# Optimization experiments

Hardware: AMD Instinct MI355X
Metric: run time of the kernel (lower is better)

## Reference

```python
import jax, jax.numpy as jnp
import numpy as np

N = 50000
E = 800000
IN_DIM = 128
HIDDEN = 128
OUT_DIM = 64
NUM_GRAPHS = 64


def setup_inputs() -> dict:
    key = jax.random.key(0)
    ks = jax.random.split(key, 16)
    x = jax.random.normal(ks[0], (N, IN_DIM), dtype=jnp.float32)
    edge_index = jax.random.randint(ks[1], (2, E), 0, N, dtype=jnp.int32)
    batch = jnp.sort(jax.random.randint(ks[2], (N,), 0, NUM_GRAPHS, dtype=jnp.int32))

    def glorot(k, shape):
        fan_in = shape[1]
        return jax.random.normal(k, shape, dtype=jnp.float32) / jnp.sqrt(jnp.float32(fan_in))

    # SAGEConv params: lin_l (on aggregated neighbors, with bias), lin_r (on self, no bias)
    return {
        "x": x,
        "edge_index": edge_index,
        "batch": batch,
        "W1l": glorot(ks[3], (HIDDEN, IN_DIM)), "b1l": jnp.zeros((HIDDEN,), jnp.float32),
        "W1r": glorot(ks[4], (HIDDEN, IN_DIM)),
        "W2l": glorot(ks[5], (HIDDEN, HIDDEN)), "b2l": jnp.zeros((HIDDEN,), jnp.float32),
        "W2r": glorot(ks[6], (HIDDEN, HIDDEN)),
        "W3l": glorot(ks[7], (HIDDEN, HIDDEN)), "b3l": jnp.zeros((HIDDEN,), jnp.float32),
        "W3r": glorot(ks[8], (HIDDEN, HIDDEN)),
        "Wlin": glorot(ks[9], (OUT_DIM, HIDDEN)), "blin": jnp.zeros((OUT_DIM,), jnp.float32),
    }


def sage_conv(x, src, dst, Wl, bl, Wr):
    # aggr='add': scatter-add source features onto target nodes, then two linears.
    agg = jax.ops.segment_sum(x[src], dst, num_segments=N)  # [N, d_in]
    return agg @ Wl.T + bl + x @ Wr.T


def reference(x, edge_index, batch, W1l, b1l, W1r, W2l, b2l, W2r, W3l, b3l, W3r, Wlin, blin):
    src, dst = edge_index[0], edge_index[1]
    h = jax.nn.relu(sage_conv(x, src, dst, W1l, b1l, W1r))
    # dropout p=0.3 is identity at inference
    h = jax.nn.relu(sage_conv(h, src, dst, W2l, b2l, W2r))
    h = sage_conv(h, src, dst, W3l, b3l, W3r)
    # global mean pool over graphs
    sums = jax.ops.segment_sum(h, batch, num_segments=NUM_GRAPHS)  # [G, hidden]
    counts = jax.ops.segment_sum(jnp.ones((N,), h.dtype), batch, num_segments=NUM_GRAPHS)
    pooled = sums / jnp.maximum(counts, 1.0)[:, None]
    return pooled @ Wlin.T + blin  # [G, out_dim]
```

## Files before the change

### kernel.cpp

```cpp
#include <hip/hip_runtime.h>


typedef __bf16 bf16x8 __attribute__((ext_vector_type(8)));
typedef float f32x4 __attribute__((ext_vector_type(4)));
typedef float f32x2 __attribute__((ext_vector_type(2)));

#define BINB 160
#define NBMAX 512

static __device__ __forceinline__ unsigned short f2bf(float f) {
    unsigned u = __builtin_bit_cast(unsigned, f);
    return (unsigned short)((u + 0x7fffu + ((u >> 16) & 1u)) >> 16);
}
static __device__ __forceinline__ uint2 pk8_fp8(const float* f) {
    int lo = 0, hi = 0;
    lo = __builtin_amdgcn_cvt_pk_fp8_f32(f[0], f[1], lo, false);
    lo = __builtin_amdgcn_cvt_pk_fp8_f32(f[2], f[3], lo, true);
    hi = __builtin_amdgcn_cvt_pk_fp8_f32(f[4], f[5], hi, false);
    hi = __builtin_amdgcn_cvt_pk_fp8_f32(f[6], f[7], hi, true);
    return make_uint2((unsigned)lo, (unsigned)hi);
}
static __device__ __forceinline__ unsigned char f2fp8(float v) {
    return (unsigned char)(__builtin_amdgcn_cvt_pk_fp8_f32(v, v, 0, false) & 0xff);
}

__global__ __launch_bounds__(256) void k_bincast(
    const int* __restrict__ ei, int* __restrict__ cnt_mat, int E, int nb, int epb,
    const float* __restrict__ x, unsigned short* __restrict__ xb,
    unsigned char* __restrict__ x8, int n8, int nxblk,
    const float* __restrict__ W1l, const float* __restrict__ W1r,
    const float* __restrict__ W2l, const float* __restrict__ W2r,
    unsigned short* __restrict__ Whi,
    const int* __restrict__ batch, unsigned* __restrict__ cnt, int nsp, int hepb)
{
    __shared__ int lc[NBMAX];
    int bid = blockIdx.x;
    if (bid < BINB) {
        for (int i = threadIdx.x; i < nb; i += 256) lc[i] = 0;
        __syncthreads();
        int b0 = bid * epb;
        int b1 = min(b0 + epb, E);
        for (int i = b0 + threadIdx.x; i < b1; i += 256)
            atomicAdd(&lc[ei[E + i] >> 7], 1);
        __syncthreads();
        for (int i = threadIdx.x; i < nb; i += 256)
            cnt_mat[i * BINB + bid] = lc[i];
    } else if (bid < BINB + nxblk) {
        int i = (bid - BINB) * 256 + threadIdx.x;
        if (i >= n8) return;
        float f[8];
        *(float4*)(f + 0) = *(const float4*)(x + (size_t)i * 8);
        *(float4*)(f + 4) = *(const float4*)(x + (size_t)i * 8 + 4);
        ushort4 oa, ob;
        oa.x = f2bf(f[0]); oa.y = f2bf(f[1]); oa.z = f2bf(f[2]); oa.w = f2bf(f[3]);
        ob.x = f2bf(f[4]); ob.y = f2bf(f[5]); ob.z = f2bf(f[6]); ob.w = f2bf(f[7]);
        int node = i >> 4, c = i & 15;
        size_t dstb = (size_t)(node >> 4) * 2048 + (size_t)(c >> 2) * 512
                    + (size_t)((c & 3) * 16 + (node & 15)) * 8;
        *(ushort4*)(xb + dstb) = oa;
        *(ushort4*)(xb + dstb + 4) = ob;
        *(uint2*)(x8 + (size_t)i * 8) = pk8_fp8(f);
    } else if (bid < BINB + nxblk + 256) {
        int wb = bid - BINB - nxblk;
        int layer = wb >> 7;
        int j = wb & 127;
        int k = threadIdx.x;
        const float* Wl = (layer == 0) ? W1l : W2l;
        const float* Wr = (layer == 0) ? W1r : W2r;
        float w = (k < 128) ? Wl[j * 128 + k] : Wr[j * 128 + k - 128];
        int js = j >> 4, mr = j & 15;
        int s = k >> 5, quad = (k >> 3) & 3, e = k & 7;
        size_t o = (size_t)layer * 32768
                 + ((size_t)(js * 8 + s) * 64 + quad * 16 + mr) * 8 + e;
        Whi[o] = f2bf(w);
    } else {
        int hb = bid - BINB - nxblk - 256;
        int b0 = hb * hepb;
        int b1 = min(b0 + hepb, E);
        for (int i = b0 + threadIdx.x; i < b1; i += 256) {
            int s = ei[i];
            int d = ei[E + i];
            int g = batch[d];
            atomicAdd(&cnt[(size_t)g * nsp + s], 1u);
        }
    }
}

__global__ __launch_bounds__(256) void k_mrowscan(
    const int* __restrict__ cnt_mat, int* __restrict__ rowloc, int* __restrict__ btot)
{
    __shared__ int s[256];
    int b = blockIdx.x;
    int t = threadIdx.x;
    int v = (t < BINB) ? cnt_mat[b * BINB + t] : 0;
    s[t] = v;
    __syncthreads();
#pragma unroll
    for (int off = 1; off < 256; off <<= 1) {
        int u = (t >= off) ? s[t - off] : 0;
        __syncthreads();
        s[t] += u;
        __syncthreads();
    }
    if (t < BINB) rowloc[b * BINB + t] = s[t] - v;
    if (t == 255) btot[b] = s[255];
}

__global__ __launch_bounds__(256) void k_scan2b(
    const int* __restrict__ btot, int* __restrict__ bbase, int nb, int* __restrict__ total_out)
{
    __shared__ int s[256];
    int t = threadIdx.x;
    int per = (nb + 255) / 256;
    int s0 = t * per, e0 = min(s0 + per, nb);
    int sum = 0;
    for (int i = s0; i < e0; ++i) sum += btot[i];
    s[t] = sum;
    __syncthreads();
#pragma unroll
    for (int off = 1; off < 256; off <<= 1) {
        int u = (t >= off) ? s[t - off] : 0;
        __syncthreads();
        s[t] += u;
        __syncthreads();
    }
    int run = s[t] - sum;
    for (int i = s0; i < e0; ++i) { bbase[i] = run; run += btot[i]; }
    if (t == 255) *total_out = s[255];
}

__global__ __launch_bounds__(256) void k_binscatter(
    const int* __restrict__ ei, const int* __restrict__ rowloc, const int* __restrict__ bbase,
    unsigned* __restrict__ binned, int E, int nb, int epb)
{
    __shared__ int lofs[NBMAX];
    __shared__ int lcnt[NBMAX];
    for (int i = threadIdx.x; i < nb; i += 256) {
        lofs[i] = rowloc[i * BINB + blockIdx.x] + bbase[i];
        lcnt[i] = 0;
    }
    __syncthreads();
    int b0 = blockIdx.x * epb;
    int b1 = min(b0 + epb, E);
    for (int i = b0 + threadIdx.x; i < b1; i += 256) {
        int s = ei[i];
        int d = ei[E + i];
        int b = d >> 7;
        int r = atomicAdd(&lcnt[b], 1);
        binned[lofs[b] + r] = (unsigned)s | ((unsigned)(d & 127) << 16);
    }
}

__global__ __launch_bounds__(256) void k_fillfine2(
    const unsigned* __restrict__ binned, const int* __restrict__ bbase,
    const int* __restrict__ batch, int* __restrict__ starts,
    unsigned short* __restrict__ csr_src, int* __restrict__ gestart,
    int E, int nb, int n)
{
    __shared__ int lc[128];
    __shared__ int lpos[128];
    int b = blockIdx.x;
    int t = threadIdx.x;
    int node0 = b << 7;
    int bs = bbase[b];
    int be = (b == nb - 1) ? E : bbase[b + 1];
    if (t < 128) lc[t] = 0;
    __syncthreads();
    for (int i = bs + t; i < be; i += 256)
        atomicAdd(&lc[(binned[i] >> 16) & 127], 1);
    __syncthreads();
    int v = (t < 128) ? lc[t] : 0;
    if (t < 128) lpos[t] = v;
    __syncthreads();
#pragma unroll
    for (int off = 1; off < 128; off <<= 1) {
        int u = (t >= off && t < 128) ? lpos[t - off] : 0;
        __syncthreads();
        if (t < 128) lpos[t] += u;
        __syncthreads();
    }
    int excl = (t < 128) ? (lpos[t] - v) : 0;
    __syncthreads();
    if (t < 128) {
        int node = node0 + t;
        if (node < n) {
            int st = bs + excl;
            starts[node] = st;
            int bc = batch[node];
            int bp = (node == 0) ? -1 : batch[node - 1];
            for (int g = bp + 1; g <= bc; ++g) gestart[g] = st;
            if (node == n - 1)
                for (int g = bc + 1; g <= 64; ++g) gestart[g] = E;
        }
        lpos[t] = bs + excl;
    }
    if (b == nb - 1 && t == 0) starts[n] = E;
    __syncthreads();
    for (int i = bs + t; i < be; i += 256) {
        unsigned e = binned[i];
        int slot = atomicAdd(&lpos[(e >> 16) & 127], 1);
        csr_src[slot] = (unsigned short)(e & 0xffffu);
    }
}

#define ACC8P(v)                                                        \
    do {                                                                \
        f32x2 p0 = __builtin_amdgcn_cvt_pk_f32_fp8((v).x, false);       \
        f32x2 p1 = __builtin_amdgcn_cvt_pk_f32_fp8((v).x, true);        \
        f32x2 p2 = __builtin_amdgcn_cvt_pk_f32_fp8((v).y, false);       \
        f32x2 p3 = __builtin_amdgcn_cvt_pk_f32_fp8((v).y, true);        \
        A01 += p0; A23 += p1; A45 += p2; A67 += p3;                     \
    } while (0)

#define PROC_CHUNK(idxv, cntv)                                          \
    {                                                                   \
        int j = 0;                                                      \
        for (; j + 16 <= (cntv); j += 16) {                             \
            int s0 = __shfl((int)(idxv), j + eg);                       \
            int s1 = __shfl((int)(idxv), j + 4 + eg);                   \
            int s2 = __shfl((int)(idxv), j + 8 + eg);                   \
            int s3 = __shfl((int)(idxv), j + 12 + eg);                  \
            uint2 v0 = *(const uint2*)(hrow + (size_t)s0 * 128);        \
            uint2 v1 = *(const uint2*)(hrow + (size_t)s1 * 128);        \
            uint2 v2 = *(const uint2*)(hrow + (size_t)s2 * 128);        \
            uint2 v3 = *(const uint2*)(hrow + (size_t)s3 * 128);        \
            ACC8P(v0);                                                  \
            ACC8P(v1);                                                  \
            ACC8P(v2);                                                  \
            ACC8P(v3);                                                  \
        }                                                               \
        for (; j + 4 <= (cntv); j += 4) {                               \
            int s0 = __shfl((int)(idxv), j + eg);                       \
            uint2 v0 = *(const uint2*)(hrow + (size_t)s0 * 128);        \
            ACC8P(v0);                                                  \
        }                                                               \
        if (j < (cntv)) {                                               \
            int k = j + eg;                                             \
            int sm = __shfl((int)(idxv), (k < (cntv)) ? k : ((cntv) - 1)); \
            uint2 v = *(const uint2*)(hrow + (size_t)sm * 128);         \
            if (k >= (cntv)) v = make_uint2(0u, 0u);                    \
            ACC8P(v);                                                   \
        }                                                               \
    }

#define REDUCE8()                                                       \
    a0 += __shfl_xor(a0, 16); a0 += __shfl_xor(a0, 32);                 \
    a1 += __shfl_xor(a1, 16); a1 += __shfl_xor(a1, 32);                 \
    a2 += __shfl_xor(a2, 16); a2 += __shfl_xor(a2, 32);                 \
    a3 += __shfl_xor(a3, 16); a3 += __shfl_xor(a3, 32);                 \
    a4 += __shfl_xor(a4, 16); a4 += __shfl_xor(a4, 32);                 \
    a5 += __shfl_xor(a5, 16); a5 += __shfl_xor(a5, 32);                 \
    a6 += __shfl_xor(a6, 16); a6 += __shfl_xor(a6, 32);                 \
    a7 += __shfl_xor(a7, 16); a7 += __shfl_xor(a7, 32);

__global__ __launch_bounds__(256) void k_layer(
    const unsigned char* __restrict__ h8_in, const int* __restrict__ starts,
    const unsigned short* __restrict__ csr, const unsigned short* __restrict__ hf,
    const unsigned short* __restrict__ Whi, const float* __restrict__ bl,
    unsigned short* __restrict__ outf, unsigned char* __restrict__ out8,
    unsigned char* __restrict__ h2t,
    int n, int nsp, int do_outf, int do_h2t)
{
    __shared__ unsigned short sagg[2048];
    int t = threadIdx.x;
    int wv = t >> 6;
    int lane = t & 63;
    int node0 = blockIdx.x * 16;

    {
        int eg = lane >> 4;
        int fb = lane & 15;
        const unsigned char* hrow = h8_in + fb * 8;
        int nodeA = node0 + wv * 4;
        int st[5];
#pragma unroll
        for (int r = 0; r < 5; ++r) {
            int nn = nodeA + r;
            st[r] = starts[nn > n ? n : nn];
        }
        unsigned idx4[4];
#pragma unroll
        for (int r = 0; r < 4; ++r)
            idx4[r] = (st[r] + lane < st[r + 1]) ? (unsigned)csr[st[r] + lane] : 0u;

#pragma unroll
        for (int r = 0; r < 4; ++r) {
            int node = nodeA + r;
            if (node >= n) break;
            f32x2 A01 = (f32x2){0.f, 0.f}, A23 = (f32x2){0.f, 0.f},
                  A45 = (f32x2){0.f, 0.f}, A67 = (f32x2){0.f, 0.f};
            int deg = st[r + 1] - st[r];
            int c0 = min(64, deg);
            PROC_CHUNK(idx4[r], c0)
            for (int base = st[r] + 64; base < st[r + 1]; base += 64) {
                int cnt2 = min(64, st[r + 1] - base);
                unsigned idx = (base + lane < st[r + 1]) ? (unsigned)csr[base + lane] : 0u;
                PROC_CHUNK(idx, cnt2)
            }
            float a0 = A01.x, a1 = A01.y, a2 = A23.x, a3 = A23.y,
                  a4 = A45.x, a5 = A45.y, a6 = A67.x, a7 = A67.y;
            REDUCE8()
            if (eg == 0) {
                int ln = node - node0;
                unsigned u0 = (unsigned)f2bf(a0) | ((unsigned)f2bf(a1) << 16);
                unsigned u1 = (unsigned)f2bf(a2) | ((unsigned)f2bf(a3) << 16);
                unsigned u2 = (unsigned)f2bf(a4) | ((unsigned)f2bf(a5) << 16);
                unsigned u3 = (unsigned)f2bf(a6) | ((unsigned)f2bf(a7) << 16);
                size_t dst = (size_t)(fb >> 2) * 512 + (size_t)((fb & 3) * 16 + ln) * 8;
                *(uint4*)(sagg + dst) = make_uint4(u0, u1, u2, u3);
            }
        }
    }
    __syncthreads();

    int quad = lane >> 4;
    int mr = lane & 15;
    int js0 = wv * 2;

    f32x4 acc0 = (f32x4){0.f, 0.f, 0.f, 0.f};
    f32x4 acc1 = (f32x4){0.f, 0.f, 0.f, 0.f};

    const unsigned short* wp = Whi + (size_t)js0 * 4096 + (size_t)lane * 8;
    const unsigned short* sa = sagg + (size_t)lane * 8;
    const unsigned short* ha = hf + (size_t)blockIdx.x * 2048 + (size_t)lane * 8;

    uint4 pb[2][3];
#define LAYER_LOAD(s, b)                                                  \
    do {                                                                  \
        pb[b][0] = *(const uint4*)(wp + (size_t)(s) * 512);               \
        pb[b][1] = *(const uint4*)(wp + 4096 + (size_t)(s) * 512);        \
        pb[b][2] = ((s) < 4)                                              \
            ? *(const uint4*)(sa + (size_t)(s) * 512)                     \
            : *(const uint4*)(ha + (size_t)((s) - 4) * 512);              \
    } while (0)

    LAYER_LOAD(0, 0);
    LAYER_LOAD(1, 1);
#pragma unroll
    for (int s = 0; s < 8; ++s) {
        int b = s & 1;
        bf16x8 bh0 = __builtin_bit_cast(bf16x8, pb[b][0]);
        bf16x8 bh1 = __builtin_bit_cast(bf16x8, pb[b][1]);
        bf16x8 A0 = __builtin_bit_cast(bf16x8, pb[b][2]);
        acc0 = __builtin_amdgcn_mfma_f32_16x16x32_bf16(A0, bh0, acc0, 0, 0, 0);
        acc1 = __builtin_amdgcn_mfma_f32_16x16x32_bf16(A0, bh1, acc1, 0, 0, 0);
        if (s + 2 < 8) LAYER_LOAD(s + 2, b);
    }
#undef LAYER_LOAD

#pragma unroll
    for (int mi = 0; mi < 2; ++mi) {
        f32x4 a = mi ? acc1 : acc0;
        int col = (js0 + mi) * 16 + mr;
        float bias = bl[col];
        int q2 = (col >> 3) & 3;
        int e2 = col & 7;
        int so = col >> 5;
        float vr[4];
#pragma unroll
        for (int r = 0; r < 4; ++r) {
            int node = node0 + quad * 4 + r;
            float v = a[r] + bias;
            v = fmaxf(v, 0.f);
            vr[r] = (node < n) ? v : 0.f;
            if (node < n) {
                if (do_outf)
                    outf[(size_t)(node >> 4) * 2048 + (size_t)so * 512
                         + (size_t)(q2 * 16 + (node & 15)) * 8 + e2] = f2bf(v);
                out8[(size_t)node * 128 + col] = f2fp8(v);
            }
        }
        if (do_h2t) {
            int pk = __builtin_amdgcn_cvt_pk_fp8_f32(vr[0], vr[1], 0, false);
            pk = __builtin_amdgcn_cvt_pk_fp8_f32(vr[2], vr[3], pk, true);
            *(unsigned*)(h2t + (size_t)col * nsp + node0 + quad * 4) = (unsigned)pk;
        }
    }
}

__global__ __launch_bounds__(256) void k_gsum(
    const unsigned* __restrict__ cnt, const unsigned char* __restrict__ h2t,
    const unsigned char* __restrict__ h8, const int* __restrict__ batch,
    float* __restrict__ gsumE, float* __restrict__ gsumP,
    int n, int nsp, int ksteps, int gb)
{
    int t = threadIdx.x;
    if ((int)blockIdx.x >= gb) {
        int wave = ((blockIdx.x - gb) * 256 + t) >> 6;
        int lane = t & 63;
        int r0 = wave * 16;
        if (r0 >= n) return;
        int r1 = min(r0 + 16, n);
        int cur = batch[r0];
        float ax = 0.f, ay = 0.f;
        for (int i = r0; i < r1; ++i) {
            int g = batch[i];
            uchar2 v = *(const uchar2*)(h8 + (size_t)i * 128 + lane * 2);
            if (g != cur) {
                atomicAdd(&gsumP[cur * 128 + lane * 2], ax);
                atomicAdd(&gsumP[cur * 128 + lane * 2 + 1], ay);
                ax = 0.f; ay = 0.f; cur = g;
            }
            unsigned pk = (unsigned)v.x | ((unsigned)v.y << 8);
            f32x2 p = __builtin_amdgcn_cvt_pk_f32_fp8((int)pk, false);
            ax += p.x;
            ay += p.y;
        }
        atomicAdd(&gsumP[cur * 128 + lane * 2], ax);
        atomicAdd(&gsumP[cur * 128 + lane * 2 + 1], ay);
        return;
    }

    int wv = t >> 6;
    int lane = t & 63;
    int fast = lane & 15;
    int kc = (lane >> 4) * 8;
    int kpb = (ksteps + gb - 1) / gb;
    int k0 = blockIdx.x * kpb, k1 = min(k0 + kpb, ksteps);
    if (k0 >= k1) return;

    f32x4 acc[8];
#pragma unroll
    for (int i = 0; i < 8; ++i) acc[i] = (f32x4){0.f, 0.f, 0.f, 0.f};

    const unsigned* ap = cnt + (size_t)(wv * 16 + fast) * nsp + kc;
    const unsigned char* bp = h2t + (size_t)fast * nsp + kc;

    for (int ks = k0; ks < k1; ++ks) {
        int kb = ks * 32;
        uint4 c0 = *(const uint4*)(ap + kb);
        uint4 c1 = *(const uint4*)(ap + kb + 4);
        unsigned q0 = (unsigned)f2bf((float)c0.x) | ((unsigned)f2bf((float)c0.y) << 16);
        unsigned q1 = (unsigned)f2bf((float)c0.z) | ((unsigned)f2bf((float)c0.w) << 16);
        unsigned q2 = (unsigned)f2bf((float)c1.x) | ((unsigned)f2bf((float)c1.y) << 16);
        unsigned q3 = (unsigned)f2bf((float)c1.z) | ((unsigned)f2bf((float)c1.w) << 16);
        uint4 au = make_uint4(q0, q1, q2, q3);
        bf16x8 af = __builtin_bit_cast(bf16x8, au);
#pragma unroll
        for (int ft = 0; ft < 8; ++ft) {
            uint2 bb = *(const uint2*)(bp + (size_t)ft * 16 * nsp + kb);
            f32x2 p0 = __builtin_amdgcn_cvt_pk_f32_fp8(bb.x, false);
            f32x2 p1 = __builtin_amdgcn_cvt_pk_f32_fp8(bb.x, true);
            f32x2 p2 = __builtin_amdgcn_cvt_pk_f32_fp8(bb.y, false);
            f32x2 p3 = __builtin_amdgcn_cvt_pk_f32_fp8(bb.y, true);
            unsigned b0 = (unsigned)f2bf(p0.x) | ((unsigned)f2bf(p0.y) << 16);
            unsigned b1 = (unsigned)f2bf(p1.x) | ((unsigned)f2bf(p1.y) << 16);
            unsigned b2 = (unsigned)f2bf(p2.x) | ((unsigned)f2bf(p2.y) << 16);
            unsigned b3 = (unsigned)f2bf(p3.x) | ((unsigned)f2bf(p3.y) << 16);
            uint4 bu = make_uint4(b0, b1, b2, b3);
            bf16x8 bf = __builtin_bit_cast(bf16x8, bu);
            acc[ft] = __builtin_amdgcn_mfma_f32_16x16x32_bf16(af, bf, acc[ft], 0, 0, 0);
        }
    }

    int quad = lane >> 4;
    int mr = lane & 15;
    int gg = wv * 16 + quad * 4;
#pragma unroll
    for (int ft = 0; ft < 8; ++ft) {
        int col = ft * 16 + mr;
#pragma unroll
        for (int r = 0; r < 4; ++r)
            atomicAdd(&gsumE[(size_t)(gg + r) * 128 + col], acc[ft][r]);
    }
}

__global__ __launch_bounds__(128) void k_final(
    const float* __restrict__ gsumE, const float* __restrict__ gsumP,
    const int* __restrict__ batch,
    const float* __restrict__ W3l, const float* __restrict__ b3,
    const float* __restrict__ W3r,
    const float* __restrict__ Wlin, const float* __restrict__ blin,
    float* __restrict__ out, int n)
{
    __shared__ float tmp[128];
    int g = blockIdx.x;
    int t = threadIdx.x;
    int lo = 0, hi = n;
    while (lo < hi) { int m = (lo + hi) >> 1; if (batch[m] < g) lo = m + 1; else hi = m; }
    int lb = lo;
    hi = n;
    while (lo < hi) { int m = (lo + hi) >> 1; if (batch[m] < g + 1) lo = m + 1; else hi = m; }
    int cnt = lo - lb;
    float inv = (cnt > 0) ? 1.f / (float)cnt : 0.f;

    float acc = 0.f;
    for (int k = 0; k < 128; ++k)
        acc += gsumE[g * 128 + k] * W3l[t * 128 + k]
             + gsumP[g * 128 + k] * W3r[t * 128 + k];
    tmp[t] = acc * inv + ((cnt > 0) ? b3[t] : 0.f);
    __syncthreads();

    if (t < 64) {
        float o = 0.f;
        for (int k = 0; k < 128; ++k)
            o += tmp[k] * Wlin[t * 128 + k];
        out[g * 64 + t] = o + blin[t];
    }
}

extern "C" void kernel_launch(void* const* d_in, const int* in_sizes, int n_in,
                              void* d_out, int out_size, void* d_ws, size_t ws_size,
                              hipStream_t stream) {
    const float* x     = (const float*)d_in[0];
    const int*   ei    = (const int*)d_in[1];
    const int*   batch = (const int*)d_in[2];
    const float* W1l = (const float*)d_in[3];
    const float* b1l = (const float*)d_in[4];
    const float* W1r = (const float*)d_in[5];
    const float* W2l = (const float*)d_in[6];
    const float* b2l = (const float*)d_in[7];
    const float* W2r = (const float*)d_in[8];
    const float* W3l = (const float*)d_in[9];
    const float* b3l = (const float*)d_in[10];
    const float* W3r = (const float*)d_in[11];
    const float* Wlin = (const float*)d_in[12];
    const float* blin = (const float*)d_in[13];

    const int N = in_sizes[2];
    const int E = in_sizes[1] / 2;
    const int nb = (N + 127) >> 7;
    const int epb = (E + BINB - 1) / BINB;
    const int NSP = ((N + 16 + 31) / 32) * 32;
    const int KSTEPS = NSP / 32;

    size_t off = 0;
    auto alloc = [&](size_t bytes) {
        void* p = (char*)d_ws + off;
        off += (bytes + 255) & ~(size_t)255;
        return p;
    };
    int* csr_start = (int*)alloc((size_t)(N + 1) * 4);
    int* cnt_mat   = (int*)alloc((size_t)nb * BINB * 4);
    int* rowloc    = (int*)alloc((size_t)nb * BINB * 4);
    int* btot      = (int*)alloc((size_t)NBMAX * 4);
    int* bbase     = (int*)alloc((size_t)NBMAX * 4);
    int* gestart   = (int*)alloc(256 + 64);
    unsigned short* csr_src = (unsigned short*)alloc((size_t)E * 2);
    unsigned*       binned  = (unsigned*)alloc((size_t)E * 4);
    unsigned short* x_bf = (unsigned short*)alloc((size_t)N * 128 * 2 + 65536);
    unsigned short* hA   = (unsigned short*)alloc((size_t)N * 128 * 2 + 65536);
    unsigned char*  x8   = (unsigned char*)alloc((size_t)N * 128);
    unsigned char*  h1_8 = (unsigned char*)alloc((size_t)N * 128);
    unsigned char*  h2_8 = (unsigned char*)alloc((size_t)N * 128);
    unsigned char*  h2T  = (unsigned char*)alloc((size_t)128 * NSP);
    unsigned short* Whi = (unsigned short*)alloc(2 * 128 * 256 * 2);
    unsigned* cnt  = (unsigned*)alloc((size_t)64 * NSP * 4);
    float* gsumE = (float*)alloc((size_t)64 * 128 * 4);
    float* gsumP = (float*)alloc((size_t)64 * 128 * 4);
    (void)ws_size;

    hipMemsetAsync(cnt, 0, (size_t)64 * NSP * 4 + (size_t)2 * 64 * 128 * 4, stream);

    int n8 = N * 128 / 8;
    int nxblk = (n8 + 255) / 256;
    const int HISTB = 256;
    int hepb = (E + HISTB - 1) / HISTB;
    k_bincast<<<BINB + nxblk + 256 + HISTB, 256, 0, stream>>>(
        ei, cnt_mat, E, nb, epb,
        x, x_bf, x8, n8, nxblk, W1l, W1r, W2l, W2r, Whi,
        batch, cnt, NSP, hepb);
    k_mrowscan<<<nb, 256, 0, stream>>>(cnt_mat, rowloc, btot);
    k_scan2b<<<1, 256, 0, stream>>>(btot, bbase, nb, csr_start + N);
    k_binscatter<<<BINB, 256, 0, stream>>>(ei, rowloc, bbase, binned, E, nb, epb);
    k_fillfine2<<<nb, 256, 0, stream>>>(binned, bbase, batch, csr_start, csr_src,
                                        gestart, E, nb, N);

    int lay_grid  = (N + 15) / 16;
    int lay2_grid = NSP / 16;
    int pool_grid = (((N + 15) / 16) + 3) / 4;
    const int GB = 256;

    k_layer<<<lay_grid, 256, 0, stream>>>(x8, csr_start, csr_src, x_bf,
                                          Whi, b1l, hA, h1_8, h2T, N, NSP, 1, 0);
    k_layer<<<lay2_grid, 256, 0, stream>>>(h1_8, csr_start, csr_src, hA,
                                           Whi + 32768, b2l, hA, h2_8, h2T, N, NSP, 0, 1);
    k_gsum<<<GB + pool_grid, 256, 0, stream>>>(cnt, h2T, h2_8, batch,
                                               gsumE, gsumP, N, NSP, KSTEPS, GB);

    k_final<<<64, 128, 0, stream>>>(gsumE, gsumP, batch, W3l, b3l, W3r,
                                    Wlin, blin, (float*)d_out, N);
}
```

Baseline: 288.1 us.

## Build graph-pool count matrix in LDS histograms and fold self-pool into bf16 GEMM

Replaces the global-atomic (graph, source) edge histogram with a per-graph, per-chunk LDS histogram kernel that reads the sorted CSR and writes bf16 counts directly. It also adds a one-hot batch matrix, so the self-feature pooling becomes a second MFMA in the same GEMM. Layer outputs are staged through shared memory for coalesced stores, and layer 2 now writes bf16 transposed features. The pooling GEMM prefetches operands and writes per-block partials, which the final kernel reduces instead of using float atomics. This removes the memset and global atomics but adds a 128xNSP bf16 count buffer, a larger partials buffer, and a serial reduction over 128 partials in the final kernel.

```diff
diff --git a/kernel.cpp b/kernel.cpp
--- a/kernel.cpp
+++ b/kernel.cpp
@@ -7,6 +7,7 @@
 
 #define BINB 160
 #define NBMAX 512
+#define CH 8192
 
 static __device__ __forceinline__ unsigned short f2bf(float f) {
     unsigned u = __builtin_bit_cast(unsigned, f);
@@ -30,8 +31,7 @@
     unsigned char* __restrict__ x8, int n8, int nxblk,
     const float* __restrict__ W1l, const float* __restrict__ W1r,
     const float* __restrict__ W2l, const float* __restrict__ W2r,
-    unsigned short* __restrict__ Whi,
-    const int* __restrict__ batch, unsigned* __restrict__ cnt, int nsp, int hepb)
+    unsigned short* __restrict__ Whi)
 {
     __shared__ int lc[NBMAX];
     int bid = blockIdx.x;
@@ -60,7 +60,7 @@
         *(ushort4*)(xb + dstb) = oa;
         *(ushort4*)(xb + dstb + 4) = ob;
         *(uint2*)(x8 + (size_t)i * 8) = pk8_fp8(f);
-    } else if (bid < BINB + nxblk + 256) {
+    } else {
         int wb = bid - BINB - nxblk;
         int layer = wb >> 7;
         int j = wb & 127;
@@ -73,16 +73,6 @@
         size_t o = (size_t)layer * 32768
                  + ((size_t)(js * 8 + s) * 64 + quad * 16 + mr) * 8 + e;
         Whi[o] = f2bf(w);
-    } else {
-        int hb = bid - BINB - nxblk - 256;
-        int b0 = hb * hepb;
-        int b1 = min(b0 + hepb, E);
-        for (int i = b0 + threadIdx.x; i < b1; i += 256) {
-            int s = ei[i];
-            int d = ei[E + i];
-            int g = batch[d];
-            atomicAdd(&cnt[(size_t)g * nsp + s], 1u);
-        }
     }
 }
 
@@ -200,6 +190,42 @@
         unsigned e = binned[i];
         int slot = atomicAdd(&lpos[(e >> 16) & 127], 1);
         csr_src[slot] = (unsigned short)(e & 0xffffu);
+    }
+}
+
+__global__ __launch_bounds__(256) void k_hist(
+    const unsigned short* __restrict__ csr, const int* __restrict__ gestart,
+    const int* __restrict__ batch, unsigned short* __restrict__ cntb,
+    int n, int nsp, int nch)
+{
+    __shared__ unsigned lc[CH];
+    int bid = blockIdx.x;
+    int c = bid % nch;
+    int gr = bid / nch;
+    int s0 = c * CH;
+    int t = threadIdx.x;
+    if (gr < 64) {
+        for (int i = t; i < CH; i += 256) lc[i] = 0;
+        __syncthreads();
+        int e0 = gestart[gr], e1 = gestart[gr + 1];
+        for (int i = e0 + t; i < e1; i += 256) {
+            unsigned d = (unsigned)((int)csr[i] - s0);
+            if (d < (unsigned)CH) atomicAdd(&lc[d], 1u);
+        }
+        __syncthreads();
+        for (int i = t; i < CH; i += 256) {
+            int s = s0 + i;
+            if (s < nsp)
+                cntb[(size_t)gr * nsp + s] = f2bf((float)lc[i]);
+        }
+    } else {
+        int g2 = gr - 64;
+        for (int i = t; i < CH; i += 256) {
+            int s = s0 + i;
+            if (s < nsp)
+                cntb[(size_t)gr * nsp + s] =
+                    (s < n && batch[s] == g2) ? (unsigned short)0x3f80 : (unsigned short)0;
+        }
     }
 }
 
@@ -258,10 +284,11 @@
     const unsigned short* __restrict__ csr, const unsigned short* __restrict__ hf,
     const unsigned short* __restrict__ Whi, const float* __restrict__ bl,
     unsigned short* __restrict__ outf, unsigned char* __restrict__ out8,
-    unsigned char* __restrict__ h2t,
-    int n, int nsp, int do_outf, int do_h2t)
+    unsigned short* __restrict__ h2tb,
+    int n, int nsp, int mode)
 {
     __shared__ unsigned short sagg[2048];
+    __shared__ unsigned char s8[2048];
     int t = threadIdx.x;
     int wv = t >> 6;
     int lane = t & 63;
@@ -348,134 +375,137 @@
     }
 #undef LAYER_LOAD
 
+    float vv[2][4];
 #pragma unroll
     for (int mi = 0; mi < 2; ++mi) {
         f32x4 a = mi ? acc1 : acc0;
         int col = (js0 + mi) * 16 + mr;
         float bias = bl[col];
-        int q2 = (col >> 3) & 3;
-        int e2 = col & 7;
-        int so = col >> 5;
-        float vr[4];
 #pragma unroll
         for (int r = 0; r < 4; ++r) {
             int node = node0 + quad * 4 + r;
-            float v = a[r] + bias;
-            v = fmaxf(v, 0.f);
-            vr[r] = (node < n) ? v : 0.f;
-            if (node < n) {
-                if (do_outf)
-                    outf[(size_t)(node >> 4) * 2048 + (size_t)so * 512
-                         + (size_t)(q2 * 16 + (node & 15)) * 8 + e2] = f2bf(v);
-                out8[(size_t)node * 128 + col] = f2fp8(v);
+            float v = fmaxf(a[r] + bias, 0.f);
+            vv[mi][r] = (node < n) ? v : 0.f;
+        }
+    }
+    __syncthreads();
+    if (mode == 0) {
+#pragma unroll
+        for (int mi = 0; mi < 2; ++mi) {
+            int col = (js0 + mi) * 16 + mr;
+            int so = col >> 5, q2 = (col >> 3) & 3, e2 = col & 7;
+#pragma unroll
+            for (int r = 0; r < 4; ++r) {
+                int nl = quad * 4 + r;
+                sagg[so * 512 + (q2 * 16 + nl) * 8 + e2] = f2bf(vv[mi][r]);
+                s8[nl * 128 + col] = f2fp8(vv[mi][r]);
             }
         }
-        if (do_h2t) {
-            int pk = __builtin_amdgcn_cvt_pk_fp8_f32(vr[0], vr[1], 0, false);
-            pk = __builtin_amdgcn_cvt_pk_fp8_f32(vr[2], vr[3], pk, true);
-            *(unsigned*)(h2t + (size_t)col * nsp + node0 + quad * 4) = (unsigned)pk;
-        }
+        __syncthreads();
+        *(uint4*)(outf + (size_t)blockIdx.x * 2048 + (size_t)t * 8) =
+            *(const uint4*)(sagg + (size_t)t * 8);
+        int nl = t >> 4;
+        if (node0 + nl < n)
+            *(uint2*)(out8 + (size_t)(node0 + nl) * 128 + (t & 15) * 8) =
+                *(const uint2*)(s8 + nl * 128 + (t & 15) * 8);
+    } else {
+#pragma unroll
+        for (int mi = 0; mi < 2; ++mi) {
+            int col = (js0 + mi) * 16 + mr;
+#pragma unroll
+            for (int r = 0; r < 4; ++r)
+                sagg[col * 16 + quad * 4 + r] = f2bf(vv[mi][r]);
+        }
+        __syncthreads();
+        int col = t >> 1;
+        *(uint4*)(h2tb + (size_t)col * nsp + node0 + (t & 1) * 8) =
+            *(const uint4*)(sagg + col * 16 + (t & 1) * 8);
     }
 }
 
 __global__ __launch_bounds__(256) void k_gsum(
-    const unsigned* __restrict__ cnt, const unsigned char* __restrict__ h2t,
-    const unsigned char* __restrict__ h8, const int* __restrict__ batch,
-    float* __restrict__ gsumE, float* __restrict__ gsumP,
-    int n, int nsp, int ksteps, int gb)
+    const unsigned short* __restrict__ cntb, const unsigned short* __restrict__ h2tb,
+    float* __restrict__ part, int nsp, int ksteps, int gb)
 {
     int t = threadIdx.x;
-    if ((int)blockIdx.x >= gb) {
-        int wave = ((blockIdx.x - gb) * 256 + t) >> 6;
-        int lane = t & 63;
-        int r0 = wave * 16;
-        if (r0 >= n) return;
-        int r1 = min(r0 + 16, n);
-        int cur = batch[r0];
-        float ax = 0.f, ay = 0.f;
-        for (int i = r0; i < r1; ++i) {
-            int g = batch[i];
-            uchar2 v = *(const uchar2*)(h8 + (size_t)i * 128 + lane * 2);
-            if (g != cur) {
-                atomicAdd(&gsumP[cur * 128 + lane * 2], ax);
-                atomicAdd(&gsumP[cur * 128 + lane * 2 + 1], ay);
-                ax = 0.f; ay = 0.f; cur = g;
-            }
-            unsigned pk = (unsigned)v.x | ((unsigned)v.y << 8);
-            f32x2 p = __builtin_amdgcn_cvt_pk_f32_fp8((int)pk, false);
-            ax += p.x;
-            ay += p.y;
-        }
-        atomicAdd(&gsumP[cur * 128 + lane * 2], ax);
-        atomicAdd(&gsumP[cur * 128 + lane * 2 + 1], ay);
-        return;
-    }
-
-    int wv = t >> 6;
-    int lane = t & 63;
+    int wv = t >> 6, lane = t & 63;
     int fast = lane & 15;
     int kc = (lane >> 4) * 8;
     int kpb = (ksteps + gb - 1) / gb;
     int k0 = blockIdx.x * kpb, k1 = min(k0 + kpb, ksteps);
-    if (k0 >= k1) return;
-
-    f32x4 acc[8];
-#pragma unroll
-    for (int i = 0; i < 8; ++i) acc[i] = (f32x4){0.f, 0.f, 0.f, 0.f};
-
-    const unsigned* ap = cnt + (size_t)(wv * 16 + fast) * nsp + kc;
-    const unsigned char* bp = h2t + (size_t)fast * nsp + kc;
-
-    for (int ks = k0; ks < k1; ++ks) {
-        int kb = ks * 32;
-        uint4 c0 = *(const uint4*)(ap + kb);
-        uint4 c1 = *(const uint4*)(ap + kb + 4);
-        unsigned q0 = (unsigned)f2bf((float)c0.x) | ((unsigned)f2bf((float)c0.y) << 16);
-        unsigned q1 = (unsigned)f2bf((float)c0.z) | ((unsigned)f2bf((float)c0.w) << 16);
-        unsigned q2 = (unsigned)f2bf((float)c1.x) | ((unsigned)f2bf((float)c1.y) << 16);
-        unsigned q3 = (unsigned)f2bf((float)c1.z) | ((unsigned)f2bf((float)c1.w) << 16);
-        uint4 au = make_uint4(q0, q1, q2, q3);
-        bf16x8 af = __builtin_bit_cast(bf16x8, au);
-#pragma unroll
-        for (int ft = 0; ft < 8; ++ft) {
-            uint2 bb = *(const uint2*)(bp + (size_t)ft * 16 * nsp + kb);
-            f32x2 p0 = __builtin_amdgcn_cvt_pk_f32_fp8(bb.x, false);
-            f32x2 p1 = __builtin_amdgcn_cvt_pk_f32_fp8(bb.x, true);
-            f32x2 p2 = __builtin_amdgcn_cvt_pk_f32_fp8(bb.y, false);
-            f32x2 p3 = __builtin_amdgcn_cvt_pk_f32_fp8(bb.y, true);
-            unsigned b0 = (unsigned)f2bf(p0.x) | ((unsigned)f2bf(p0.y) << 16);
-            unsigned b1 = (unsigned)f2bf(p1.x) | ((unsigned)f2bf(p1.y) << 16);
-            unsigned b2 = (unsigned)f2bf(p2.x) | ((unsigned)f2bf(p2.y) << 16);
-            unsigned b3 = (unsigned)f2bf(p3.x) | ((unsigned)f2bf(p3.y) << 16);
-            uint4 bu = make_uint4(b0, b1, b2, b3);
-            bf16x8 bf = __builtin_bit_cast(bf16x8, bu);
-            acc[ft] = __builtin_amdgcn_mfma_f32_16x16x32_bf16(af, bf, acc[ft], 0, 0, 0);
-        }
-    }
-
-    int quad = lane >> 4;
-    int mr = lane & 15;
-    int gg = wv * 16 + quad * 4;
+
+    f32x4 accE[8], accP[8];
+#pragma unroll
+    for (int i = 0; i < 8; ++i) {
+        accE[i] = (f32x4){0.f, 0.f, 0.f, 0.f};
+        accP[i] = (f32x4){0.f, 0.f, 0.f, 0.f};
+    }
+
+    const unsigned short* apE = cntb + (size_t)(wv * 16 + fast) * nsp + kc;
+    const unsigned short* apP = apE + (size_t)64 * nsp;
+    const unsigned short* bp  = h2tb + (size_t)fast * nsp + kc;
+
+    if (k0 < k1) {
+        int kb = k0 * 32;
+        uint4 ca0 = *(const uint4*)(apE + kb);
+        uint4 ca1 = *(const uint4*)(apP + kb);
+        uint4 cb[8];
+#pragma unroll
+        for (int ft = 0; ft < 8; ++ft)
+            cb[ft] = *(const uint4*)(bp + (size_t)ft * 16 * nsp + kb);
+        for (int ks = k0; ks < k1; ++ks) {
+            int kn = min(ks + 1, k1 - 1) * 32;
+            uint4 na0 = *(const uint4*)(apE + kn);
+            uint4 na1 = *(const uint4*)(apP + kn);
+            uint4 nb[8];
+#pragma unroll
+            for (int ft = 0; ft < 8; ++ft)
+                nb[ft] = *(const uint4*)(bp + (size_t)ft * 16 * nsp + kn);
+            bf16x8 aE = __builtin_bit_cast(bf16x8, ca0);
+            bf16x8 aP = __builtin_bit_cast(bf16x8, ca1);
+#pragma unroll
+            for (int ft = 0; ft < 8; ++ft) {
+                bf16x8 bf = __builtin_bit_cast(bf16x8, cb[ft]);
+                accE[ft] = __builtin_amdgcn_mfma_f32_16x16x32_bf16(aE, bf, accE[ft], 0, 0, 0);
+                accP[ft] = __builtin_amdgcn_mfma_f32_16x16x32_bf16(aP, bf, accP[ft], 0, 0, 0);
+            }
+            ca0 = na0; ca1 = na1;
+#pragma unroll
+            for (int ft = 0; ft < 8; ++ft) cb[ft] = nb[ft];
+        }
+    }
+    float* po = part + (size_t)blockIdx.x * 16384;
+    int quad = lane >> 4, mr = lane & 15;
 #pragma unroll
     for (int ft = 0; ft < 8; ++ft) {
         int col = ft * 16 + mr;
 #pragma unroll
-        for (int r = 0; r < 4; ++r)
-            atomicAdd(&gsumE[(size_t)(gg + r) * 128 + col], acc[ft][r]);
+        for (int r = 0; r < 4; ++r) {
+            po[(size_t)(wv * 16 + quad * 4 + r) * 128 + col] = accE[ft][r];
+            po[(size_t)(64 + wv * 16 + quad * 4 + r) * 128 + col] = accP[ft][r];
+        }
     }
 }
 
 __global__ __launch_bounds__(128) void k_final(
-    const float* __restrict__ gsumE, const float* __restrict__ gsumP,
-    const int* __restrict__ batch,
+    const float* __restrict__ part, const int* __restrict__ batch,
     const float* __restrict__ W3l, const float* __restrict__ b3,
     const float* __restrict__ W3r,
     const float* __restrict__ Wlin, const float* __restrict__ blin,
-    float* __restrict__ out, int n)
-{
-    __shared__ float tmp[128];
+    float* __restrict__ out, int n, int gb)
+{
+    __shared__ float sE[128], sP[128], tmp[128];
     int g = blockIdx.x;
     int t = threadIdx.x;
+    float se = 0.f, sp = 0.f;
+    for (int p = 0; p < gb; ++p) {
+        const float* pp = part + (size_t)p * 16384;
+        se += pp[g * 128 + t];
+        sp += pp[(64 + g) * 128 + t];
+    }
+    sE[t] = se;
+    sP[t] = sp;
+
     int lo = 0, hi = n;
     while (lo < hi) { int m = (lo + hi) >> 1; if (batch[m] < g) lo = m + 1; else hi = m; }
     int lb = lo;
@@ -483,11 +513,11 @@
     while (lo < hi) { int m = (lo + hi) >> 1; if (batch[m] < g + 1) lo = m + 1; else hi = m; }
     int cnt = lo - lb;
     float inv = (cnt > 0) ? 1.f / (float)cnt : 0.f;
+    __syncthreads();
 
     float acc = 0.f;
     for (int k = 0; k < 128; ++k)
-        acc += gsumE[g * 128 + k] * W3l[t * 128 + k]
-             + gsumP[g * 128 + k] * W3r[t * 128 + k];
+        acc += sE[k] * W3l[t * 128 + k] + sP[k] * W3r[t * 128 + k];
     tmp[t] = acc * inv + ((cnt > 0) ? b3[t] : 0.f);
     __syncthreads();
 
@@ -521,8 +551,10 @@
     const int E = in_sizes[1] / 2;
     const int nb = (N + 127) >> 7;
     const int epb = (E + BINB - 1) / BINB;
-    const int NSP = ((N + 16 + 31) / 32) * 32;
+    const int NSP = ((N + 31) / 32) * 32;
     const int KSTEPS = NSP / 32;
+    const int NCH = (NSP + CH - 1) / CH;
+    const int GB = 128;
 
     size_t off = 0;
     auto alloc = [&](size_t bytes) {
@@ -542,42 +574,33 @@
     unsigned short* hA   = (unsigned short*)alloc((size_t)N * 128 * 2 + 65536);
     unsigned char*  x8   = (unsigned char*)alloc((size_t)N * 128);
     unsigned char*  h1_8 = (unsigned char*)alloc((size_t)N * 128);
-    unsigned char*  h2_8 = (unsigned char*)alloc((size_t)N * 128);
-    unsigned char*  h2T  = (unsigned char*)alloc((size_t)128 * NSP);
-    unsigned short* Whi = (unsigned short*)alloc(2 * 128 * 256 * 2);
-    unsigned* cnt  = (unsigned*)alloc((size_t)64 * NSP * 4);
-    float* gsumE = (float*)alloc((size_t)64 * 128 * 4);
-    float* gsumP = (float*)alloc((size_t)64 * 128 * 4);
+    unsigned short* h2Tb = (unsigned short*)alloc((size_t)128 * NSP * 2);
+    unsigned short* cntb = (unsigned short*)alloc((size_t)128 * NSP * 2);
+    unsigned short* Whi  = (unsigned short*)alloc(2 * 128 * 256 * 2);
+    float*          part = (float*)alloc((size_t)GB * 16384 * 4);
     (void)ws_size;
-
-    hipMemsetAsync(cnt, 0, (size_t)64 * NSP * 4 + (size_t)2 * 64 * 128 * 4, stream);
 
     int n8 = N * 128 / 8;
     int nxblk = (n8 + 255) / 256;
-    const int HISTB = 256;
-    int hepb = (E + HISTB - 1) / HISTB;
-    k_bincast<<<BINB + nxblk + 256 + HISTB, 256, 0, stream>>>(
+    k_bincast<<<BINB + nxblk + 256, 256, 0, stream>>>(
         ei, cnt_mat, E, nb, epb,
-        x, x_bf, x8, n8, nxblk, W1l, W1r, W2l, W2r, Whi,
-        batch, cnt, NSP, hepb);
+        x, x_bf, x8, n8, nxblk, W1l, W1r, W2l, W2r, Whi);
     k_mrowscan<<<nb, 256, 0, stream>>>(cnt_mat, rowloc, btot);
     k_scan2b<<<1, 256, 0, stream>>>(btot, bbase, nb, csr_start + N);
     k_binscatter<<<BINB, 256, 0, stream>>>(ei, rowloc, bbase, binned, E, nb, epb);
     k_fillfine2<<<nb, 256, 0, stream>>>(binned, bbase, batch, csr_start, csr_src,
                                         gestart, E, nb, N);
+    k_hist<<<128 * NCH, 256, 0, stream>>>(csr_src, gestart, batch, cntb, N, NSP, NCH);
 
     int lay_grid  = (N + 15) / 16;
     int lay2_grid = NSP / 16;
-    int pool_grid = (((N + 15) / 16) + 3) / 4;
-    const int GB = 256;
 
     k_layer<<<lay_grid, 256, 0, stream>>>(x8, csr_start, csr_src, x_bf,
-                                          Whi, b1l, hA, h1_8, h2T, N, NSP, 1, 0);
+                                          Whi, b1l, hA, h1_8, h2Tb, N, NSP, 0);
     k_layer<<<lay2_grid, 256, 0, stream>>>(h1_8, csr_start, csr_src, hA,
-                                           Whi + 32768, b2l, hA, h2_8, h2T, N, NSP, 0, 1);
-    k_gsum<<<GB + pool_grid, 256, 0, stream>>>(cnt, h2T, h2_8, batch,
-                                               gsumE, gsumP, N, NSP, KSTEPS, GB);
-
-    k_final<<<64, 128, 0, stream>>>(gsumE, gsumP, batch, W3l, b3l, W3r,
-                                    Wlin, blin, (float*)d_out, N);
-}
+                                           Whi + 32768, b2l, hA, h1_8, h2Tb, N, NSP, 1);
+    k_gsum<<<GB, 256, 0, stream>>>(cntb, h2Tb, part, NSP, KSTEPS, GB);
+
+    k_final<<<64, 128, 0, stream>>>(part, batch, W3l, b3l, W3r,
+                                    Wlin, blin, (float*)d_out, N, GB);
+}
```

Measured after the change: 275.7 us. -4.3%, faster.
